# Optimization experiments

Hardware: AMD Instinct MI355X
Metric: run time of the kernel (lower is better)

## Reference

```python
import jax, jax.numpy as jnp
import numpy as np

VOCAB, EMB, HIDDEN, OUT = 50000, 300, 512, 2
SEQ, BATCH = 512, 1024


def setup_inputs() -> dict:
    key = jax.random.key(0)
    k_text, k_len, k_emb, k_w1, k_b1, k_w2, k_b2 = jax.random.split(key, 7)
    text = jax.random.randint(k_text, (SEQ, BATCH), 1, VOCAB, dtype=jnp.int64 if jax.config.jax_enable_x64 else jnp.int32)
    lengths = jax.random.randint(k_len, (BATCH,), 1, SEQ + 1, dtype=text.dtype)
    emb_table = jax.random.normal(k_emb, (VOCAB, EMB), dtype=jnp.float32) * 0.1
    emb_table = emb_table.at[0].set(0.0)  # padding_idx=0 row zeroed like nn.Embedding
    W1 = jax.random.normal(k_w1, (EMB, HIDDEN), dtype=jnp.float32) * (1.0 / np.sqrt(EMB))
    b1 = jax.random.normal(k_b1, (HIDDEN,), dtype=jnp.float32) * 0.01
    W2 = jax.random.normal(k_w2, (HIDDEN, OUT), dtype=jnp.float32) * (1.0 / np.sqrt(HIDDEN))
    b2 = jax.random.normal(k_b2, (OUT,), dtype=jnp.float32) * 0.01
    return {"text": text, "lengths": lengths, "emb_table": emb_table,
            "W1": W1, "b1": b1, "W2": W2, "b2": b2}


def reference(text, lengths, emb_table, W1, b1, W2, b2):
    # text: [S, B] int; embedding lookup -> [S, B, E]
    embedded = emb_table[text]
    # masked mean over the first `lengths[b]` tokens (vectorized segment mean)
    seq = embedded.shape[0]
    mask = (jnp.arange(seq)[:, None] < lengths[None, :]).astype(embedded.dtype)  # [S, B]
    pooled = jnp.einsum('sbe,sb->be', embedded, mask) / lengths[:, None].astype(embedded.dtype)  # [B, E]
    # fc1 -> (dropout p=0, identity) -> relu -> fc2
    h = jax.nn.relu(pooled @ W1 + b1)
    return h @ W2 + b2
```

## Files before the change

kernel.cpp:

```cpp
#include <hip/hip_runtime.h>

constexpr int EMB    = 300;
constexpr int EMB4   = 75;
constexpr int HIDDEN = 512;
constexpr int SEQ    = 512;
constexpr int BATCH  = 1024;
constexpr int VOCAB  = 50000;
constexpr int NBUK   = 32;
constexpr int BDIV   = 1563;
constexpr int PB     = 4;
constexpr int GFC1   = 16;

__device__ __forceinline__ float4 f4add(float4 a, float4 b) {
    return make_float4(a.x + b.x, a.y + b.y, a.z + b.z, a.w + b.w);
}

__global__ __launch_bounds__(256) void bucketize_kernel(
    const int* __restrict__ text,
    const int* __restrict__ lengths,
    int* __restrict__ btok,
    int* __restrict__ boff)
{
    const int wave = threadIdx.x >> 6;
    const int lane = threadIdx.x & 63;
    const int b    = blockIdx.x * 4 + wave;
    const int len  = lengths[b];
    const unsigned long long ltmask = (1ull << lane) - 1ull;

    int cnt = 0;
#pragma unroll
    for (int c = 0; c < 8; ++c) {
        const int s = c * 64 + lane;
        int k = NBUK;
        if (s < len) k = text[(size_t)s * BATCH + b] / BDIV;
        for (int kk = 0; kk < NBUK; ++kk) {
            const unsigned long long m = __ballot(k == kk);
            if (lane == kk) cnt += __popcll(m);
        }
    }
    int incl = cnt;
#pragma unroll
    for (int off = 1; off < 32; off <<= 1) {
        const int v = __shfl_up(incl, off);
        if (lane >= off && lane < NBUK) incl += v;
    }
    const int excl = incl - cnt;
    if (lane < NBUK)  boff[b * (NBUK + 1) + lane] = excl;
    if (lane == NBUK - 1) boff[b * (NBUK + 1) + NBUK] = incl;

    int base = excl;
#pragma unroll
    for (int c = 0; c < 8; ++c) {
        const int s = c * 64 + lane;
        int tok = 0, k = NBUK;
        if (s < len) { tok = text[(size_t)s * BATCH + b]; k = tok / BDIV; }
        unsigned long long mym = 0;
        int chunkcnt = 0;
        for (int kk = 0; kk < NBUK; ++kk) {
            const unsigned long long m = __ballot(k == kk);
            if (k == kk) mym = m;
            if (lane == kk) chunkcnt = __popcll(m);
        }
        const int rank = __popcll(mym & ltmask);
        const int pos  = __shfl(base, k) + rank;
        if (s < len) btok[(size_t)b * SEQ + pos] = tok;
        base += chunkcnt;
    }
}

__global__ __launch_bounds__(320) void pool_kernel(
    const int* __restrict__ btok,
    const int* __restrict__ boff,
    const float* __restrict__ emb,
    float* __restrict__ partial,
    int NX)
{
    const int x  = blockIdx.x % NX;
    const int b0 = (blockIdx.x / NX) * PB;
    const int NJ = NBUK / NX;

    __shared__ int toks[PB][SEQ];
    __shared__ int seg[PB][2];

    if (threadIdx.x < PB) {
        const int b  = b0 + threadIdx.x;
        const int lo = boff[b * (NBUK + 1) + x * NJ];
        const int hi = boff[b * (NBUK + 1) + x * NJ + NJ];
        seg[threadIdx.x][0] = lo;
        seg[threadIdx.x][1] = hi - lo;
    }
    __syncthreads();

    for (int g = 0; g < PB; ++g) {
        const int lo = seg[g][0], n = seg[g][1];
        for (int t = threadIdx.x; t < n; t += 320)
            toks[g][t] = btok[(size_t)(b0 + g) * SEQ + lo + t];
    }
    __syncthreads();

    const int g = threadIdx.x / 80;
    const int c = threadIdx.x % 80;
    if (c < EMB4) {
        const int n = seg[g][1];
        float4 A = make_float4(0.f, 0.f, 0.f, 0.f);
        float4 B = A;
        int i = 0;
        for (; i + 8 <= n; i += 8) {
            const int t0 = toks[g][i + 0];
            const int t1 = toks[g][i + 1];
            const int t2 = toks[g][i + 2];
            const int t3 = toks[g][i + 3];
            const int t4 = toks[g][i + 4];
            const int t5 = toks[g][i + 5];
            const int t6 = toks[g][i + 6];
            const int t7 = toks[g][i + 7];
            const float4 v0 = ((const float4*)(emb + (size_t)t0 * EMB))[c];
            const float4 v1 = ((const float4*)(emb + (size_t)t1 * EMB))[c];
            const float4 v2 = ((const float4*)(emb + (size_t)t2 * EMB))[c];
            const float4 v3 = ((const float4*)(emb + (size_t)t3 * EMB))[c];
            const float4 v4 = ((const float4*)(emb + (size_t)t4 * EMB))[c];
            const float4 v5 = ((const float4*)(emb + (size_t)t5 * EMB))[c];
            const float4 v6 = ((const float4*)(emb + (size_t)t6 * EMB))[c];
            const float4 v7 = ((const float4*)(emb + (size_t)t7 * EMB))[c];
            A = f4add(A, f4add(f4add(v0, v1), f4add(v2, v3)));
            B = f4add(B, f4add(f4add(v4, v5), f4add(v6, v7)));
        }
        for (; i + 4 <= n; i += 4) {
            const float4 v0 = ((const float4*)(emb + (size_t)toks[g][i + 0] * EMB))[c];
            const float4 v1 = ((const float4*)(emb + (size_t)toks[g][i + 1] * EMB))[c];
            const float4 v2 = ((const float4*)(emb + (size_t)toks[g][i + 2] * EMB))[c];
            const float4 v3 = ((const float4*)(emb + (size_t)toks[g][i + 3] * EMB))[c];
            A = f4add(A, f4add(f4add(v0, v1), f4add(v2, v3)));
        }
        for (; i < n; ++i)
            B = f4add(B, ((const float4*)(emb + (size_t)toks[g][i] * EMB))[c]);
        A = f4add(A, B);
        ((float4*)(partial + ((size_t)x * BATCH + b0 + g) * EMB))[c] = A;
    }
}

template<int NX>
__global__ __launch_bounds__(512) void fc1_kernel(
    const float* __restrict__ partial,
    const int* __restrict__ lengths,
    const float* __restrict__ W1,
    const float* __restrict__ b1,
    float* __restrict__ hbuf)
{
    __shared__ float4 pQ[GFC1 / 4][EMB];
    const int b0  = blockIdx.x * GFC1;
    const int tid = threadIdx.x;

    float* pQf = (float*)pQ;
    for (int i = tid; i < EMB * GFC1; i += 512) {
        const int g = i / EMB;
        const int e = i - g * EMB;
        float s = 0.f;
#pragma unroll
        for (int xx = 0; xx < NX; ++xx)
            s += partial[((size_t)xx * BATCH + b0 + g) * EMB + e];
        pQf[((g >> 2) * EMB + e) * 4 + (g & 3)] = s / (float)lengths[b0 + g];
    }
    __syncthreads();

    const int j  = blockIdx.y * 128 + (tid & 127);
    const int gs = tid >> 7;
    const float bias = b1[j];
    float4 acc = make_float4(bias, bias, bias, bias);

    for (int e = 0; e < EMB; e += 10) {
        const float w0 = W1[(size_t)(e + 0) * HIDDEN + j];
        const float w1 = W1[(size_t)(e + 1) * HIDDEN + j];
        const float w2 = W1[(size_t)(e + 2) * HIDDEN + j];
        const float w3 = W1[(size_t)(e + 3) * HIDDEN + j];
        const float w4 = W1[(size_t)(e + 4) * HIDDEN + j];
        const float w5 = W1[(size_t)(e + 5) * HIDDEN + j];
        const float w6 = W1[(size_t)(e + 6) * HIDDEN + j];
        const float w7 = W1[(size_t)(e + 7) * HIDDEN + j];
        const float w8 = W1[(size_t)(e + 8) * HIDDEN + j];
        const float w9 = W1[(size_t)(e + 9) * HIDDEN + j];
        const float4 p0 = pQ[gs][e + 0];
        const float4 p1 = pQ[gs][e + 1];
        const float4 p2 = pQ[gs][e + 2];
        const float4 p3 = pQ[gs][e + 3];
        const float4 p4 = pQ[gs][e + 4];
        const float4 p5 = pQ[gs][e + 5];
        const float4 p6 = pQ[gs][e + 6];
        const float4 p7 = pQ[gs][e + 7];
        const float4 p8 = pQ[gs][e + 8];
        const float4 p9 = pQ[gs][e + 9];
        acc.x += p0.x * w0 + p1.x * w1 + p2.x * w2 + p3.x * w3 + p4.x * w4
               + p5.x * w5 + p6.x * w6 + p7.x * w7 + p8.x * w8 + p9.x * w9;
        acc.y += p0.y * w0 + p1.y * w1 + p2.y * w2 + p3.y * w3 + p4.y * w4
               + p5.y * w5 + p6.y * w6 + p7.y * w7 + p8.y * w8 + p9.y * w9;
        acc.z += p0.z * w0 + p1.z * w1 + p2.z * w2 + p3.z * w3 + p4.z * w4
               + p5.z * w5 + p6.z * w6 + p7.z * w7 + p8.z * w8 + p9.z * w9;
        acc.w += p0.w * w0 + p1.w * w1 + p2.w * w2 + p3.w * w3 + p4.w * w4
               + p5.w * w5 + p6.w * w6 + p7.w * w7 + p8.w * w8 + p9.w * w9;
    }
    const int bb = b0 + gs * 4;
    hbuf[(size_t)(bb + 0) * HIDDEN + j] = fmaxf(acc.x, 0.f);
    hbuf[(size_t)(bb + 1) * HIDDEN + j] = fmaxf(acc.y, 0.f);
    hbuf[(size_t)(bb + 2) * HIDDEN + j] = fmaxf(acc.z, 0.f);
    hbuf[(size_t)(bb + 3) * HIDDEN + j] = fmaxf(acc.w, 0.f);
}

__global__ __launch_bounds__(256) void fc2_kernel(
    const float* __restrict__ hbuf,
    const float* __restrict__ W2,
    const float* __restrict__ b2,
    float* __restrict__ out)
{
    const int wave = threadIdx.x >> 6;
    const int lane = threadIdx.x & 63;
    const int b    = blockIdx.x * 4 + wave;

    const float4* hrow = (const float4*)(hbuf + (size_t)b * HIDDEN);
    const float4* W2v  = (const float4*)W2;
    float s0 = 0.f, s1 = 0.f;
#pragma unroll
    for (int q = 0; q < 2; ++q) {
        const int c = lane + q * 64;
        const float4 h  = hrow[c];
        const float4 wA = W2v[2 * c + 0];
        const float4 wB = W2v[2 * c + 1];
        s0 += h.x * wA.x + h.y * wA.z + h.z * wB.x + h.w * wB.z;
        s1 += h.x * wA.y + h.y * wA.w + h.z * wB.y + h.w * wB.w;
    }
#pragma unroll
    for (int off = 32; off > 0; off >>= 1) {
        s0 += __shfl_down(s0, off);
        s1 += __shfl_down(s1, off);
    }
    if (lane == 0) {
        out[b * 2 + 0] = s0 + b2[0];
        out[b * 2 + 1] = s1 + b2[1];
    }
}

extern "C" void kernel_launch(void* const* d_in, const int* in_sizes, int n_in,
                              void* d_out, int out_size, void* d_ws, size_t ws_size,
                              hipStream_t stream) {
    const int*   text    = (const int*)d_in[0];
    const int*   lengths = (const int*)d_in[1];
    const float* emb     = (const float*)d_in[2];
    const float* W1      = (const float*)d_in[3];
    const float* b1      = (const float*)d_in[4];
    const float* W2      = (const float*)d_in[5];
    const float* b2      = (const float*)d_in[6];
    float*       out     = (float*)d_out;

    char* ws = (char*)d_ws;
    const size_t btokBytes = (size_t)BATCH * SEQ * sizeof(int);
    const size_t boffBytes = (size_t)BATCH * (NBUK + 1) * sizeof(int);
    const size_t poolBytes = (size_t)BATCH * EMB * sizeof(float);
    const size_t hbufBytes = (size_t)BATCH * HIDDEN * sizeof(float);

    int*   btok = (int*)ws;
    int*   boff = (int*)(ws + btokBytes);
    float* partial = (float*)(ws + btokBytes + boffBytes);

    const size_t fixed = btokBytes + boffBytes + hbufBytes;
    int NX = 1;
    if      (ws_size >= fixed + 8 * poolBytes) NX = 8;
    else if (ws_size >= fixed + 4 * poolBytes) NX = 4;
    else if (ws_size >= fixed + 2 * poolBytes) NX = 2;
    float* hbuf = (float*)(ws + btokBytes + boffBytes + (size_t)NX * poolBytes);

    bucketize_kernel<<<BATCH / 4, 256, 0, stream>>>(text, lengths, btok, boff);
    pool_kernel<<<NX * (BATCH / PB), 320, 0, stream>>>(btok, boff, emb, partial, NX);

    dim3 fgrid(BATCH / GFC1, HIDDEN / 128);
    switch (NX) {
        case 8: fc1_kernel<8><<<fgrid, 512, 0, stream>>>(partial, lengths, W1, b1, hbuf); break;
        case 4: fc1_kernel<4><<<fgrid, 512, 0, stream>>>(partial, lengths, W1, b1, hbuf); break;
        case 2: fc1_kernel<2><<<fgrid, 512, 0, stream>>>(partial, lengths, W1, b1, hbuf); break;
        default: fc1_kernel<1><<<fgrid, 512, 0, stream>>>(partial, lengths, W1, b1, hbuf); break;
    }
    fc2_kernel<<<BATCH / 4, 256, 0, stream>>>(hbuf, W2, b2, out);
}
```

Measured before the change: 72.91 us.

## Split pooling by position range and two half-waves per batch row

The pooling kernel now divides each row's sorted token list into equal positional slices per x, using lengths, instead of slicing by vocabulary bucket. This balances work across the NX splits. It also doubles the block to 640 threads, with two thread groups per batch row handling interleaved tokens and combining their sums through shared memory. The aim is more memory-level parallelism and even load, at the cost of an extra sync and a shared-memory reduction. Slicing by position weakens the locality that vocabulary bucketing gave within each split.

```diff
diff --git a/kernel.cpp b/kernel.cpp
--- a/kernel.cpp
+++ b/kernel.cpp
@@ -68,24 +68,24 @@
     }
 }
 
-__global__ __launch_bounds__(320) void pool_kernel(
+__global__ __launch_bounds__(640) void pool_kernel(
     const int* __restrict__ btok,
-    const int* __restrict__ boff,
+    const int* __restrict__ lengths,
     const float* __restrict__ emb,
     float* __restrict__ partial,
     int NX)
 {
     const int x  = blockIdx.x % NX;
     const int b0 = (blockIdx.x / NX) * PB;
-    const int NJ = NBUK / NX;
-
-    __shared__ int toks[PB][SEQ];
-    __shared__ int seg[PB][2];
+
+    __shared__ int    toks[PB][SEQ];
+    __shared__ int    seg[PB][2];
+    __shared__ float4 red[PB * 2][EMB4 + 1];
 
     if (threadIdx.x < PB) {
-        const int b  = b0 + threadIdx.x;
-        const int lo = boff[b * (NBUK + 1) + x * NJ];
-        const int hi = boff[b * (NBUK + 1) + x * NJ + NJ];
+        const int len = lengths[b0 + threadIdx.x];
+        const int lo  = (len * x) / NX;
+        const int hi  = (len * (x + 1)) / NX;
         seg[threadIdx.x][0] = lo;
         seg[threadIdx.x][1] = hi - lo;
     }
@@ -93,27 +93,30 @@
 
     for (int g = 0; g < PB; ++g) {
         const int lo = seg[g][0], n = seg[g][1];
-        for (int t = threadIdx.x; t < n; t += 320)
+        for (int t = threadIdx.x; t < n; t += 640)
             toks[g][t] = btok[(size_t)(b0 + g) * SEQ + lo + t];
     }
     __syncthreads();
 
-    const int g = threadIdx.x / 80;
-    const int c = threadIdx.x % 80;
+    const int hg   = threadIdx.x / 80;
+    const int c    = threadIdx.x % 80;
+    const int g    = hg >> 1;
+    const int half = hg & 1;
+
     if (c < EMB4) {
         const int n = seg[g][1];
         float4 A = make_float4(0.f, 0.f, 0.f, 0.f);
         float4 B = A;
-        int i = 0;
-        for (; i + 8 <= n; i += 8) {
-            const int t0 = toks[g][i + 0];
-            const int t1 = toks[g][i + 1];
-            const int t2 = toks[g][i + 2];
-            const int t3 = toks[g][i + 3];
-            const int t4 = toks[g][i + 4];
-            const int t5 = toks[g][i + 5];
-            const int t6 = toks[g][i + 6];
-            const int t7 = toks[g][i + 7];
+        int i = half;
+        for (; i + 14 < n; i += 16) {
+            const int t0 = toks[g][i +  0];
+            const int t1 = toks[g][i +  2];
+            const int t2 = toks[g][i +  4];
+            const int t3 = toks[g][i +  6];
+            const int t4 = toks[g][i +  8];
+            const int t5 = toks[g][i + 10];
+            const int t6 = toks[g][i + 12];
+            const int t7 = toks[g][i + 14];
             const float4 v0 = ((const float4*)(emb + (size_t)t0 * EMB))[c];
             const float4 v1 = ((const float4*)(emb + (size_t)t1 * EMB))[c];
             const float4 v2 = ((const float4*)(emb + (size_t)t2 * EMB))[c];
@@ -125,17 +128,22 @@
             A = f4add(A, f4add(f4add(v0, v1), f4add(v2, v3)));
             B = f4add(B, f4add(f4add(v4, v5), f4add(v6, v7)));
         }
-        for (; i + 4 <= n; i += 4) {
+        for (; i + 6 < n; i += 8) {
             const float4 v0 = ((const float4*)(emb + (size_t)toks[g][i + 0] * EMB))[c];
-            const float4 v1 = ((const float4*)(emb + (size_t)toks[g][i + 1] * EMB))[c];
-            const float4 v2 = ((const float4*)(emb + (size_t)toks[g][i + 2] * EMB))[c];
-            const float4 v3 = ((const float4*)(emb + (size_t)toks[g][i + 3] * EMB))[c];
+            const float4 v1 = ((const float4*)(emb + (size_t)toks[g][i + 2] * EMB))[c];
+            const float4 v2 = ((const float4*)(emb + (size_t)toks[g][i + 4] * EMB))[c];
+            const float4 v3 = ((const float4*)(emb + (size_t)toks[g][i + 6] * EMB))[c];
             A = f4add(A, f4add(f4add(v0, v1), f4add(v2, v3)));
         }
-        for (; i < n; ++i)
+        for (; i < n; i += 2)
             B = f4add(B, ((const float4*)(emb + (size_t)toks[g][i] * EMB))[c]);
-        A = f4add(A, B);
-        ((float4*)(partial + ((size_t)x * BATCH + b0 + g) * EMB))[c] = A;
+        red[hg][c] = f4add(A, B);
+    }
+    __syncthreads();
+
+    if (c < EMB4 && half == 0) {
+        const float4 s = f4add(red[hg][c], red[hg + 1][c]);
+        ((float4*)(partial + ((size_t)x * BATCH + b0 + g) * EMB))[c] = s;
     }
 }
 
@@ -268,7 +276,7 @@
     float* hbuf = (float*)(ws + btokBytes + boffBytes + (size_t)NX * poolBytes);
 
     bucketize_kernel<<<BATCH / 4, 256, 0, stream>>>(text, lengths, btok, boff);
-    pool_kernel<<<NX * (BATCH / PB), 320, 0, stream>>>(btok, boff, emb, partial, NX);
+    pool_kernel<<<NX * (BATCH / PB), 640, 0, stream>>>(btok, lengths, emb, partial, NX);
 
     dim3 fgrid(BATCH / GFC1, HIDDEN / 128);
     switch (NX) {
```

Measured after the change: 80.39 us. +10.3%, slower.

## Load-balance pooling by pairing long and short sequences via length sort

Applied to the files above, without the earlier changes.

Adds a bitonic sort of batch rows by length inside the bucketize kernel, run as one extra block alongside the bucketize blocks. The pool kernel then handles one long and one short row per block with 640 threads, split into eight token groups that each walk the buckets, followed by a shared-memory reduction. It writes the final mean straight to pooled. This removes the NX-way vocabulary split, the partial buffers and the partial-sum pass in fc1, aiming to balance work across blocks and drop the extra reduction traffic. The cost is a serial single-block sort and a within-block reduction step.

```diff
diff --git a/kernel.cpp b/kernel.cpp
--- a/kernel.cpp
+++ b/kernel.cpp
@@ -5,144 +5,165 @@
 constexpr int HIDDEN = 512;
 constexpr int SEQ    = 512;
 constexpr int BATCH  = 1024;
-constexpr int VOCAB  = 50000;
 constexpr int NBUK   = 32;
 constexpr int BDIV   = 1563;
-constexpr int PB     = 4;
 constexpr int GFC1   = 16;
 
 __device__ __forceinline__ float4 f4add(float4 a, float4 b) {
     return make_float4(a.x + b.x, a.y + b.y, a.z + b.z, a.w + b.w);
 }
 
-__global__ __launch_bounds__(256) void bucketize_kernel(
+__global__ __launch_bounds__(512) void prep_kernel(
     const int* __restrict__ text,
     const int* __restrict__ lengths,
     int* __restrict__ btok,
-    int* __restrict__ boff)
-{
-    const int wave = threadIdx.x >> 6;
-    const int lane = threadIdx.x & 63;
-    const int b    = blockIdx.x * 4 + wave;
-    const int len  = lengths[b];
-    const unsigned long long ltmask = (1ull << lane) - 1ull;
-
-    int cnt = 0;
-#pragma unroll
-    for (int c = 0; c < 8; ++c) {
-        const int s = c * 64 + lane;
-        int k = NBUK;
-        if (s < len) k = text[(size_t)s * BATCH + b] / BDIV;
-        for (int kk = 0; kk < NBUK; ++kk) {
-            const unsigned long long m = __ballot(k == kk);
-            if (lane == kk) cnt += __popcll(m);
-        }
-    }
-    int incl = cnt;
-#pragma unroll
-    for (int off = 1; off < 32; off <<= 1) {
-        const int v = __shfl_up(incl, off);
-        if (lane >= off && lane < NBUK) incl += v;
-    }
-    const int excl = incl - cnt;
-    if (lane < NBUK)  boff[b * (NBUK + 1) + lane] = excl;
-    if (lane == NBUK - 1) boff[b * (NBUK + 1) + NBUK] = incl;
-
-    int base = excl;
-#pragma unroll
-    for (int c = 0; c < 8; ++c) {
-        const int s = c * 64 + lane;
-        int tok = 0, k = NBUK;
-        if (s < len) { tok = text[(size_t)s * BATCH + b]; k = tok / BDIV; }
-        unsigned long long mym = 0;
-        int chunkcnt = 0;
-        for (int kk = 0; kk < NBUK; ++kk) {
-            const unsigned long long m = __ballot(k == kk);
-            if (k == kk) mym = m;
-            if (lane == kk) chunkcnt = __popcll(m);
-        }
-        const int rank = __popcll(mym & ltmask);
-        const int pos  = __shfl(base, k) + rank;
-        if (s < len) btok[(size_t)b * SEQ + pos] = tok;
-        base += chunkcnt;
-    }
-}
-
-__global__ __launch_bounds__(320) void pool_kernel(
+    int* __restrict__ boff,
+    int* __restrict__ sortperm)
+{
+    if (blockIdx.x < 128) {
+        const int wave = threadIdx.x >> 6;
+        const int lane = threadIdx.x & 63;
+        const int b    = blockIdx.x * 8 + wave;
+        const int len  = lengths[b];
+        const unsigned long long ltmask = (1ull << lane) - 1ull;
+
+        int cnt = 0;
+#pragma unroll
+        for (int c = 0; c < 8; ++c) {
+            const int s = c * 64 + lane;
+            int k = NBUK;
+            if (s < len) k = text[(size_t)s * BATCH + b] / BDIV;
+            for (int kk = 0; kk < NBUK; ++kk) {
+                const unsigned long long m = __ballot(k == kk);
+                if (lane == kk) cnt += __popcll(m);
+            }
+        }
+        int incl = cnt;
+#pragma unroll
+        for (int off = 1; off < 32; off <<= 1) {
+            const int v = __shfl_up(incl, off);
+            if (lane >= off && lane < NBUK) incl += v;
+        }
+        const int excl = incl - cnt;
+        if (lane < NBUK)  boff[b * (NBUK + 1) + lane] = excl;
+        if (lane == NBUK - 1) boff[b * (NBUK + 1) + NBUK] = incl;
+
+        int base = excl;
+#pragma unroll
+        for (int c = 0; c < 8; ++c) {
+            const int s = c * 64 + lane;
+            int tok = 0, k = NBUK;
+            if (s < len) { tok = text[(size_t)s * BATCH + b]; k = tok / BDIV; }
+            unsigned long long mym = 0;
+            int chunkcnt = 0;
+            for (int kk = 0; kk < NBUK; ++kk) {
+                const unsigned long long m = __ballot(k == kk);
+                if (k == kk) mym = m;
+                if (lane == kk) chunkcnt = __popcll(m);
+            }
+            const int rank = __popcll(mym & ltmask);
+            const int pos  = __shfl(base, k) + rank;
+            if (s < len) btok[(size_t)b * SEQ + pos] = tok;
+            base += chunkcnt;
+        }
+    } else {
+        __shared__ int key[1024];
+        for (int i = threadIdx.x; i < 1024; i += 512)
+            key[i] = (lengths[i] << 10) | i;
+        __syncthreads();
+        for (int k = 2; k <= 1024; k <<= 1) {
+            for (int j = k >> 1; j > 0; j >>= 1) {
+                const int t = threadIdx.x;
+                const int i = ((t & ~(j - 1)) << 1) | (t & (j - 1));
+                const int p = i | j;
+                const bool up = ((i & k) == 0);
+                const int a = key[i], c = key[p];
+                if ((a > c) == up) { key[i] = c; key[p] = a; }
+                __syncthreads();
+            }
+        }
+        for (int i = threadIdx.x; i < 1024; i += 512)
+            sortperm[i] = key[i] & 1023;
+    }
+}
+
+__global__ __launch_bounds__(640) void pool_kernel(
     const int* __restrict__ btok,
     const int* __restrict__ boff,
+    const int* __restrict__ lengths,
+    const int* __restrict__ sortperm,
     const float* __restrict__ emb,
-    float* __restrict__ partial,
-    int NX)
-{
-    const int x  = blockIdx.x % NX;
-    const int b0 = (blockIdx.x / NX) * PB;
-    const int NJ = NBUK / NX;
-
-    __shared__ int toks[PB][SEQ];
-    __shared__ int seg[PB][2];
-
-    if (threadIdx.x < PB) {
-        const int b  = b0 + threadIdx.x;
-        const int lo = boff[b * (NBUK + 1) + x * NJ];
-        const int hi = boff[b * (NBUK + 1) + x * NJ + NJ];
-        seg[threadIdx.x][0] = lo;
-        seg[threadIdx.x][1] = hi - lo;
-    }
-    __syncthreads();
-
-    for (int g = 0; g < PB; ++g) {
-        const int lo = seg[g][0], n = seg[g][1];
-        for (int t = threadIdx.x; t < n; t += 320)
-            toks[g][t] = btok[(size_t)(b0 + g) * SEQ + lo + t];
-    }
-    __syncthreads();
-
-    const int g = threadIdx.x / 80;
-    const int c = threadIdx.x % 80;
+    float* __restrict__ pooled)
+{
+    __shared__ int    toksL[2][SEQ];
+    __shared__ int    boffL[2][NBUK + 1];
+    __shared__ int    binfo[4];
+    __shared__ float4 red[8][80];
+
+    const int tid = threadIdx.x;
+    const int q   = blockIdx.x;
+
+    if (tid < 2) {
+        const int b = sortperm[tid == 0 ? q : (1023 - q)];
+        binfo[tid]     = b;
+        binfo[2 + tid] = lengths[b];
+    }
+    __syncthreads();
+
+    for (int i = tid; i < 2 * (NBUK + 1); i += 640) {
+        const int g = i / (NBUK + 1), k = i - g * (NBUK + 1);
+        boffL[g][k] = boff[binfo[g] * (NBUK + 1) + k];
+    }
+    for (int g = 0; g < 2; ++g) {
+        const int n  = binfo[2 + g];
+        const int bb = binfo[g];
+        for (int t = tid; t < n; t += 640)
+            toksL[g][t] = btok[(size_t)bb * SEQ + t];
+    }
+    __syncthreads();
+
+    const int grp = tid / 80;
+    const int c   = tid % 80;
+    float4 A0 = make_float4(0.f, 0.f, 0.f, 0.f);
+    float4 A1 = A0;
+
     if (c < EMB4) {
-        const int n = seg[g][1];
-        float4 A = make_float4(0.f, 0.f, 0.f, 0.f);
-        float4 B = A;
-        int i = 0;
-        for (; i + 8 <= n; i += 8) {
-            const int t0 = toks[g][i + 0];
-            const int t1 = toks[g][i + 1];
-            const int t2 = toks[g][i + 2];
-            const int t3 = toks[g][i + 3];
-            const int t4 = toks[g][i + 4];
-            const int t5 = toks[g][i + 5];
-            const int t6 = toks[g][i + 6];
-            const int t7 = toks[g][i + 7];
-            const float4 v0 = ((const float4*)(emb + (size_t)t0 * EMB))[c];
-            const float4 v1 = ((const float4*)(emb + (size_t)t1 * EMB))[c];
-            const float4 v2 = ((const float4*)(emb + (size_t)t2 * EMB))[c];
-            const float4 v3 = ((const float4*)(emb + (size_t)t3 * EMB))[c];
-            const float4 v4 = ((const float4*)(emb + (size_t)t4 * EMB))[c];
-            const float4 v5 = ((const float4*)(emb + (size_t)t5 * EMB))[c];
-            const float4 v6 = ((const float4*)(emb + (size_t)t6 * EMB))[c];
-            const float4 v7 = ((const float4*)(emb + (size_t)t7 * EMB))[c];
-            A = f4add(A, f4add(f4add(v0, v1), f4add(v2, v3)));
-            B = f4add(B, f4add(f4add(v4, v5), f4add(v6, v7)));
-        }
-        for (; i + 4 <= n; i += 4) {
-            const float4 v0 = ((const float4*)(emb + (size_t)toks[g][i + 0] * EMB))[c];
-            const float4 v1 = ((const float4*)(emb + (size_t)toks[g][i + 1] * EMB))[c];
-            const float4 v2 = ((const float4*)(emb + (size_t)toks[g][i + 2] * EMB))[c];
-            const float4 v3 = ((const float4*)(emb + (size_t)toks[g][i + 3] * EMB))[c];
-            A = f4add(A, f4add(f4add(v0, v1), f4add(v2, v3)));
-        }
-        for (; i < n; ++i)
-            B = f4add(B, ((const float4*)(emb + (size_t)toks[g][i] * EMB))[c]);
-        A = f4add(A, B);
-        ((float4*)(partial + ((size_t)x * BATCH + b0 + g) * EMB))[c] = A;
-    }
-}
-
-template<int NX>
+        const float4* e4 = (const float4*)emb;
+        for (int k = 0; k < NBUK; ++k) {
+            int lo = boffL[0][k], hi = boffL[0][k + 1];
+            for (int p = lo + grp; p < hi; p += 8)
+                A0 = f4add(A0, e4[(size_t)toksL[0][p] * EMB4 + c]);
+            lo = boffL[1][k]; hi = boffL[1][k + 1];
+            for (int p = lo + grp; p < hi; p += 8)
+                A1 = f4add(A1, e4[(size_t)toksL[1][p] * EMB4 + c]);
+        }
+    }
+
+    red[grp][c] = A0;
+    __syncthreads();
+    if (grp == 0 && c < EMB4) {
+        float4 s = red[0][c];
+#pragma unroll
+        for (int g = 1; g < 8; ++g) s = f4add(s, red[g][c]);
+        const float inv = 1.0f / (float)binfo[2];
+        s.x *= inv; s.y *= inv; s.z *= inv; s.w *= inv;
+        ((float4*)(pooled + (size_t)binfo[0] * EMB))[c] = s;
+    }
+    __syncthreads();
+    red[grp][c] = A1;
+    __syncthreads();
+    if (grp == 0 && c < EMB4) {
+        float4 s = red[0][c];
+#pragma unroll
+        for (int g = 1; g < 8; ++g) s = f4add(s, red[g][c]);
+        const float inv = 1.0f / (float)binfo[3];
+        s.x *= inv; s.y *= inv; s.z *= inv; s.w *= inv;
+        ((float4*)(pooled + (size_t)binfo[1] * EMB))[c] = s;
+    }
+}
+
 __global__ __launch_bounds__(512) void fc1_kernel(
-    const float* __restrict__ partial,
-    const int* __restrict__ lengths,
+    const float* __restrict__ pooled,
     const float* __restrict__ W1,
     const float* __restrict__ b1,
     float* __restrict__ hbuf)
@@ -155,11 +176,7 @@
     for (int i = tid; i < EMB * GFC1; i += 512) {
         const int g = i / EMB;
         const int e = i - g * EMB;
-        float s = 0.f;
-#pragma unroll
-        for (int xx = 0; xx < NX; ++xx)
-            s += partial[((size_t)xx * BATCH + b0 + g) * EMB + e];
-        pQf[((g >> 2) * EMB + e) * 4 + (g & 3)] = s / (float)lengths[b0 + g];
+        pQf[((g >> 2) * EMB + e) * 4 + (g & 3)] = pooled[(size_t)(b0 + g) * EMB + e];
     }
     __syncthreads();
 
@@ -219,8 +236,8 @@
     const float4* W2v  = (const float4*)W2;
     float s0 = 0.f, s1 = 0.f;
 #pragma unroll
-    for (int q = 0; q < 2; ++q) {
-        const int c = lane + q * 64;
+    for (int qq = 0; qq < 2; ++qq) {
+        const int c = lane + qq * 64;
         const float4 h  = hrow[c];
         const float4 wA = W2v[2 * c + 0];
         const float4 wB = W2v[2 * c + 1];
@@ -253,29 +270,17 @@
     char* ws = (char*)d_ws;
     const size_t btokBytes = (size_t)BATCH * SEQ * sizeof(int);
     const size_t boffBytes = (size_t)BATCH * (NBUK + 1) * sizeof(int);
+    const size_t spBytes   = (size_t)BATCH * sizeof(int);
     const size_t poolBytes = (size_t)BATCH * EMB * sizeof(float);
-    const size_t hbufBytes = (size_t)BATCH * HIDDEN * sizeof(float);
-
-    int*   btok = (int*)ws;
-    int*   boff = (int*)(ws + btokBytes);
-    float* partial = (float*)(ws + btokBytes + boffBytes);
-
-    const size_t fixed = btokBytes + boffBytes + hbufBytes;
-    int NX = 1;
-    if      (ws_size >= fixed + 8 * poolBytes) NX = 8;
-    else if (ws_size >= fixed + 4 * poolBytes) NX = 4;
-    else if (ws_size >= fixed + 2 * poolBytes) NX = 2;
-    float* hbuf = (float*)(ws + btokBytes + boffBytes + (size_t)NX * poolBytes);
-
-    bucketize_kernel<<<BATCH / 4, 256, 0, stream>>>(text, lengths, btok, boff);
-    pool_kernel<<<NX * (BATCH / PB), 320, 0, stream>>>(btok, boff, emb, partial, NX);
-
-    dim3 fgrid(BATCH / GFC1, HIDDEN / 128);
-    switch (NX) {
-        case 8: fc1_kernel<8><<<fgrid, 512, 0, stream>>>(partial, lengths, W1, b1, hbuf); break;
-        case 4: fc1_kernel<4><<<fgrid, 512, 0, stream>>>(partial, lengths, W1, b1, hbuf); break;
-        case 2: fc1_kernel<2><<<fgrid, 512, 0, stream>>>(partial, lengths, W1, b1, hbuf); break;
-        default: fc1_kernel<1><<<fgrid, 512, 0, stream>>>(partial, lengths, W1, b1, hbuf); break;
-    }
+
+    int*   btok     = (int*)ws;
+    int*   boff     = (int*)(ws + btokBytes);
+    int*   sortperm = (int*)(ws + btokBytes + boffBytes);
+    float* pooled   = (float*)(ws + btokBytes + boffBytes + spBytes);
+    float* hbuf     = (float*)(ws + btokBytes + boffBytes + spBytes + poolBytes);
+
+    prep_kernel<<<129, 512, 0, stream>>>(text, lengths, btok, boff, sortperm);
+    pool_kernel<<<BATCH / 2, 640, 0, stream>>>(btok, boff, lengths, sortperm, emb, pooled);
+    fc1_kernel<<<dim3(BATCH / GFC1, HIDDEN / 128), 512, 0, stream>>>(pooled, W1, b1, hbuf);
     fc2_kernel<<<BATCH / 4, 256, 0, stream>>>(hbuf, W2, b2, out);
 }
```

New measurement: 92.02 us. 26.2% more time.
